# Kernel tuning notes

Hardware: AMD Instinct MI355X
Metric: run time of the kernel (lower is better)

## Reference

```python
import jax, jax.numpy as jnp
import numpy as np

EMBEDDING_DIM = 128
CODEBOOK_SIZE = 8192
COMMITMENT_COST = 0.25


def setup_inputs() -> dict:
    key = jax.random.key(0)
    k1, k2 = jax.random.split(key)
    inputs = jax.random.normal(k1, (8, 2048, EMBEDDING_DIM), dtype=jnp.float32)
    embeddings = jax.random.normal(k2, (EMBEDDING_DIM, CODEBOOK_SIZE), dtype=jnp.float32)
    return {"inputs": inputs, "embeddings": embeddings}


def reference(inputs, embeddings):
    # inputs: [B, T, D]; embeddings: [D, K]
    B, T, D = inputs.shape
    K = embeddings.shape[1]
    flat = inputs.reshape(-1, D)                      # [N, D]
    sim = flat @ embeddings                           # [N, K]
    dists = (jnp.sum(flat * flat, axis=1, keepdims=True)
             - 2.0 * sim
             + jnp.sum(embeddings * embeddings, axis=0, keepdims=True))
    idx_flat = jnp.argmax(-dists, axis=1)             # [N], matches tf.argmax(-d)
    encodings = jax.nn.one_hot(idx_flat, K, dtype=inputs.dtype)  # [N, K]
    encoding_indices = idx_flat.reshape(B, T)
    quantized = jnp.take(embeddings.T, encoding_indices, axis=0)  # [B, T, D]
    e_latent_loss = jnp.mean((jax.lax.stop_gradient(quantized) - inputs) ** 2)
    q_latent_loss = jnp.mean((quantized - jax.lax.stop_gradient(inputs)) ** 2)
    loss = q_latent_loss + COMMITMENT_COST * e_latent_loss
    quantized = inputs + jax.lax.stop_gradient(quantized - inputs)  # straight-through
    return quantized, encodings, encoding_indices, loss
```

## Files before the change

### kernel.cpp

```cpp
#include <hip/hip_runtime.h>

#define D 128
#define K 8192
#define N 16384
#define BM 64
#define BN 256
#define NCH (K / BN)
#define THREADS 512
#define CAND_CAP 3072
#define DELTA 0.5f
#define RMIN_INIT 0xFF800000u

typedef __attribute__((ext_vector_type(4))) float f32x4;
typedef __attribute__((ext_vector_type(16))) float f32x16;
typedef __attribute__((ext_vector_type(8))) short short8;

__device__ __forceinline__ unsigned short f2bf(float f) {
    unsigned int b = __float_as_uint(f);
    return (unsigned short)((b + 0x7FFFu + ((b >> 16) & 1u)) >> 16);
}
__device__ __forceinline__ unsigned int fsort(float f) {
    unsigned int b = __float_as_uint(f);
    return b ^ ((unsigned int)((int)b >> 31) | 0x80000000u);
}
__device__ __forceinline__ float funsort(unsigned int u) {
    return __uint_as_float((u & 0x80000000u) ? (u ^ 0x80000000u) : ~u);
}

__global__ __launch_bounds__(256) void prep_kernel(const float* __restrict__ E,
        unsigned short* __restrict__ e1t, float* __restrict__ e2t,
        float* __restrict__ enorm) {
    __shared__ float esum[8][32];
    const int t = threadIdx.x;
    const int kl = t & 31, dg = t >> 5;
    const int k = blockIdx.x * 32 + kl;
    float s = 0.f;
    __align__(16) unsigned short tmpb[16];
    __align__(16) float tmpf[16];
#pragma unroll
    for (int j = 0; j < 16; ++j) {
        float v = E[(size_t)(dg * 16 + j) * K + k];
        s += v * v;
        tmpb[j] = f2bf(v);
        tmpf[j] = v;
    }
    *(f32x4*)(e1t + (size_t)k * D + dg * 16) = *(const f32x4*)tmpb;
    *(f32x4*)(e1t + (size_t)k * D + dg * 16 + 8) = *(const f32x4*)(tmpb + 8);
    if (e2t) {
#pragma unroll
        for (int q = 0; q < 4; ++q)
            *(f32x4*)(e2t + (size_t)k * D + dg * 16 + 4 * q) = *(const f32x4*)(tmpf + 4 * q);
    }
    esum[dg][kl] = s;
    __syncthreads();
    if (t < 32) {
        float e = 0.f;
#pragma unroll
        for (int g = 0; g < 8; ++g) e += esum[g][t];
        enorm[blockIdx.x * 32 + t] = e;
    }
}

template<int E2T>
__global__ __launch_bounds__(THREADS, 2) void main_kernel(
        const float* __restrict__ X, const float* __restrict__ E,
        const unsigned short* __restrict__ e1t, const float* __restrict__ e2t,
        const float* __restrict__ enorm, float* __restrict__ out,
        float* __restrict__ partials) {
    __shared__ __align__(16) unsigned short b_s[2][BN * D];
    __shared__ unsigned long long cand[CAND_CAP];
    __shared__ unsigned long long best[BM];
    __shared__ unsigned int rmin[BM];
    __shared__ float red[THREADS];
    __shared__ int candn;

    const int t = threadIdx.x;
    const int wid = t >> 6, l = t & 63;
    const int l31 = l & 31, lh = l >> 5;
    const int wm = wid >> 2, wn = wid & 3;
    const int rowbase = blockIdx.x * BM;

    float* qout = out;
    float* enc = out + (size_t)N * D;
    float* idxout = enc + (size_t)N * K;

    if (t < BM) { rmin[t] = RMIN_INIT; best[t] = ~0ull; }
    if (t == 0) candn = 0;

    short8 afr[8];
    {
        const int row = rowbase + wm * 32 + l31;
#pragma unroll
        for (int ks = 0; ks < 8; ++ks) {
            const float* xp = X + (size_t)row * D + ks * 16 + lh * 8;
            f32x4 v0 = *(const f32x4*)xp;
            f32x4 v1 = *(const f32x4*)(xp + 4);
            short8 a;
            a[0] = (short)f2bf(v0[0]); a[1] = (short)f2bf(v0[1]);
            a[2] = (short)f2bf(v0[2]); a[3] = (short)f2bf(v0[3]);
            a[4] = (short)f2bf(v1[0]); a[5] = (short)f2bf(v1[1]);
            a[6] = (short)f2bf(v1[2]); a[7] = (short)f2bf(v1[3]);
            afr[ks] = a;
        }
    }

    f32x4 sreg[8];
    {
        const f32x4* gs = (const f32x4*)e1t;
#pragma unroll
        for (int i = 0; i < 8; ++i) sreg[i] = gs[t + THREADS * i];
#pragma unroll
        for (int i = 0; i < 8; ++i) {
            int unit = t + THREADS * i;
            int c = unit >> 4, slot = unit & 15;
            *(f32x4*)((char*)&b_s[0][0] + c * 256 + ((slot ^ (c & 15)) << 4)) = sreg[i];
        }
    }

    int cur = 0;
    for (int ch = 0; ch < NCH; ++ch) {
        if (ch + 1 < NCH) {
            const f32x4* gs = (const f32x4*)(e1t + (size_t)(ch + 1) * BN * D);
#pragma unroll
            for (int i = 0; i < 8; ++i) sreg[i] = gs[t + THREADS * i];
        }
        __syncthreads();

        float thrv[16];
#pragma unroll
        for (int q = 0; q < 4; ++q) {
            const int base = wm * 32 + 4 * lh + 8 * q;
            uint4 rv = *(const uint4*)&rmin[base];
            thrv[4 * q + 0] = funsort(rv.x);
            thrv[4 * q + 1] = funsort(rv.y);
            thrv[4 * q + 2] = funsort(rv.z);
            thrv[4 * q + 3] = funsort(rv.w);
        }

        f32x16 acc[2];
#pragma unroll
        for (int nf = 0; nf < 2; ++nf)
#pragma unroll
            for (int r = 0; r < 16; ++r) acc[nf][r] = 0.f;

#pragma unroll
        for (int ks = 0; ks < 8; ++ks) {
            short8 bf[2];
#pragma unroll
            for (int nf = 0; nf < 2; ++nf) {
                int c = wn * 64 + nf * 32 + l31;
                int slot = ks * 2 + lh;
                bf[nf] = *(const short8*)((const char*)&b_s[cur][0] + c * 256 + ((slot ^ (c & 15)) << 4));
            }
#pragma unroll
            for (int nf = 0; nf < 2; ++nf)
                acc[nf] = __builtin_amdgcn_mfma_f32_32x32x16_bf16(afr[ks], bf[nf], acc[nf], 0, 0, 0);
        }

        const int chcol = ch * BN;
        float dts[2][16];
#pragma unroll
        for (int nf = 0; nf < 2; ++nf) {
            const int col = chcol + wn * 64 + nf * 32 + l31;
            const float en = enorm[col];
#pragma unroll
            for (int r = 0; r < 16; ++r) dts[nf][r] = en - 2.f * acc[nf][r];
        }

        float cmin[16];
#pragma unroll
        for (int r = 0; r < 16; ++r) cmin[r] = fminf(dts[0][r], dts[1][r]);
#pragma unroll
        for (int m = 1; m <= 16; m <<= 1)
#pragma unroll
            for (int r = 0; r < 16; ++r)
                cmin[r] = fminf(cmin[r], __shfl_xor(cmin[r], m, 64));

#pragma unroll
        for (int r = 0; r < 16; ++r) {
            const int ro = wm * 32 + 4 * lh + 8 * (r >> 2) + (r & 3);
            const float te = fminf(thrv[r], cmin[r]) + DELTA;
#pragma unroll
            for (int nf = 0; nf < 2; ++nf) {
                if (dts[nf][r] < te) {
                    const int col = chcol + wn * 64 + nf * 32 + l31;
                    int ci = atomicAdd(&candn, 1);
                    if (ci < CAND_CAP)
                        cand[ci] = ((unsigned long long)fsort(dts[nf][r]) << 32) |
                                   ((unsigned long long)ro << 13) | (unsigned)col;
                }
            }
            if (l31 == 0 && cmin[r] < thrv[r])
                atomicMin(&rmin[ro], fsort(cmin[r]));
        }

        {
            const f32x4 z = {0.f, 0.f, 0.f, 0.f};
#pragma unroll
            for (int i = 0; i < 8; ++i) {
                int unit = t + THREADS * i;
                int row = unit >> 6, cu = unit & 63;
                __builtin_nontemporal_store(z,
                    (f32x4*)(enc + (size_t)(rowbase + row) * K + chcol + cu * 4));
            }
        }

        if (ch + 1 < NCH) {
#pragma unroll
            for (int i = 0; i < 8; ++i) {
                int unit = t + THREADS * i;
                int c = unit >> 4, slot = unit & 15;
                *(f32x4*)((char*)&b_s[cur ^ 1][0] + c * 256 + ((slot ^ (c & 15)) << 4)) = sreg[i];
            }
        }
        cur ^= 1;
    }

    __syncthreads();

    {
        int n = candn; if (n > CAND_CAP) n = CAND_CAP;
        for (int i = wid; i < n; i += 8) {
            const unsigned long long e = cand[i];
            const float dta = funsort((unsigned int)(e >> 32));
            const int ro = (int)((e >> 13) & 63u);
            const int col = (int)(e & 8191u);
            if (dta < funsort(rmin[ro]) + DELTA) {
                const int row = rowbase + ro;
                float x0 = X[(size_t)row * D + l];
                float x1 = X[(size_t)row * D + 64 + l];
                float e0, e1;
                if (E2T) {
                    e0 = e2t[(size_t)col * D + l];
                    e1 = e2t[(size_t)col * D + 64 + l];
                } else {
                    e0 = E[(size_t)l * K + col];
                    e1 = E[(size_t)(l + 64) * K + col];
                }
                float s = x0 * e0 + x1 * e1;
#pragma unroll
                for (int m = 1; m <= 32; m <<= 1) s += __shfl_xor(s, m, 64);
                if (l == 0) {
                    float dtx = enorm[col] - 2.f * s;
                    atomicMin(&best[ro],
                        ((unsigned long long)fsort(dtx) << 32) | (unsigned)col);
                }
            }
        }
    }
    __syncthreads();

    if (t < BM) {
        const int k = (int)(best[t] & 8191ull);
        idxout[rowbase + t] = (float)k;
        __builtin_nontemporal_store(1.0f, &enc[(size_t)(rowbase + t) * K + k]);
    }

    const int rr = t >> 3, sL = t & 7;
    const int row = rowbase + rr;
    const int kb = (int)(best[rr] & 8191ull);
    float part = 0.f;
#pragma unroll
    for (int j = 0; j < 4; ++j) {
        const int d0 = sL * 16 + 4 * j;
        f32x4 xv = *(const f32x4*)(X + (size_t)row * D + d0);
        f32x4 ev;
        if (E2T) {
            ev = *(const f32x4*)(e2t + (size_t)kb * D + d0);
        } else {
#pragma unroll
            for (int u = 0; u < 4; ++u) ev[u] = E[(size_t)(d0 + u) * K + kb];
        }
        f32x4 qv;
#pragma unroll
        for (int u = 0; u < 4; ++u) {
            float df = ev[u] - xv[u];
            qv[u] = xv[u] + df;
            part += df * df;
        }
        *(f32x4*)(qout + (size_t)row * D + d0) = qv;
    }
    red[t] = part;
    __syncthreads();
#pragma unroll
    for (int off = THREADS / 2; off > 0; off >>= 1) {
        if (t < off) red[t] += red[t + off];
        __syncthreads();
    }
    if (t == 0) partials[blockIdx.x] = red[0];
}

__global__ __launch_bounds__(256) void loss_kernel(const float* __restrict__ partials,
                                                   float* __restrict__ out) {
    __shared__ float red[256];
    const int t = threadIdx.x;
    red[t] = partials[t];
    __syncthreads();
    for (int off = 128; off > 0; off >>= 1) {
        if (t < off) red[t] += red[t + off];
        __syncthreads();
    }
    if (t == 0) {
        float mean = red[0] / (float)((size_t)N * D);
        out[(size_t)N * D + (size_t)N * K + N] = mean + 0.25f * mean;
    }
}

extern "C" void kernel_launch(void* const* d_in, const int* in_sizes, int n_in,
                              void* d_out, int out_size, void* d_ws, size_t ws_size,
                              hipStream_t stream) {
    const float* X = (const float*)d_in[0];
    const float* E = (const float*)d_in[1];
    float* out = (float*)d_out;
    char* ws = (char*)d_ws;

    const size_t E1T_B = (size_t)K * D * 2;
    const size_t E2T_B = (size_t)K * D * 4;
    const bool use_e2t = ws_size >= E1T_B + E2T_B + 64 * 1024;

    unsigned short* e1t = (unsigned short*)ws;
    float* e2t; float* enorm; float* partials;
    if (use_e2t) {
        e2t = (float*)(ws + E1T_B);
        enorm = (float*)(ws + E1T_B + E2T_B);
        partials = enorm + K;
    } else {
        e2t = nullptr;
        enorm = (float*)(ws + E1T_B);
        partials = enorm + K;
    }

    hipLaunchKernelGGL(prep_kernel, dim3(K / 32), dim3(256), 0, stream,
                       E, e1t, e2t, enorm);
    if (use_e2t)
        hipLaunchKernelGGL((main_kernel<1>), dim3(N / BM), dim3(THREADS), 0, stream,
                           X, E, e1t, e2t, enorm, out, partials);
    else
        hipLaunchKernelGGL((main_kernel<0>), dim3(N / BM), dim3(THREADS), 0, stream,
                           X, E, e1t, e2t, enorm, out, partials);
    hipLaunchKernelGGL(loss_kernel, dim3(1), dim3(256), 0, stream, partials, out);
}
```

Before: 200.5 us.

## Drop LDS staging of codebook; load B fragments directly from global per wave

```diff
diff --git a/kernel.cpp b/kernel.cpp
--- a/kernel.cpp
+++ b/kernel.cpp
@@ -3,11 +3,11 @@
 #define D 128
 #define K 8192
 #define N 16384
-#define BM 64
-#define BN 256
-#define NCH (K / BN)
-#define THREADS 512
-#define CAND_CAP 3072
+#define BM 32
+#define TILES 64
+#define GRP 4
+#define THREADS 256
+#define CAND_CAP 1024
 #define DELTA 0.5f
 #define RMIN_INIT 0xFF800000u
 
@@ -67,7 +67,6 @@
         const unsigned short* __restrict__ e1t, const float* __restrict__ e2t,
         const float* __restrict__ enorm, float* __restrict__ out,
         float* __restrict__ partials) {
-    __shared__ __align__(16) unsigned short b_s[2][BN * D];
     __shared__ unsigned long long cand[CAND_CAP];
     __shared__ unsigned long long best[BM];
     __shared__ unsigned int rmin[BM];
@@ -77,7 +76,7 @@
     const int t = threadIdx.x;
     const int wid = t >> 6, l = t & 63;
     const int l31 = l & 31, lh = l >> 5;
-    const int wm = wid >> 2, wn = wid & 3;
+    const int wn = wid;
     const int rowbase = blockIdx.x * BM;
 
     float* qout = out;
@@ -86,10 +85,11 @@
 
     if (t < BM) { rmin[t] = RMIN_INIT; best[t] = ~0ull; }
     if (t == 0) candn = 0;
+    __syncthreads();
 
     short8 afr[8];
     {
-        const int row = rowbase + wm * 32 + l31;
+        const int row = rowbase + l31;
 #pragma unroll
         for (int ks = 0; ks < 8; ++ks) {
             const float* xp = X + (size_t)row * D + ks * 16 + lh * 8;
@@ -104,32 +104,58 @@
         }
     }
 
-    f32x4 sreg[8];
-    {
-        const f32x4* gs = (const f32x4*)e1t;
-#pragma unroll
-        for (int i = 0; i < 8; ++i) sreg[i] = gs[t + THREADS * i];
-#pragma unroll
-        for (int i = 0; i < 8; ++i) {
-            int unit = t + THREADS * i;
-            int c = unit >> 4, slot = unit & 15;
-            *(f32x4*)((char*)&b_s[0][0] + c * 256 + ((slot ^ (c & 15)) << 4)) = sreg[i];
-        }
-    }
-
-    int cur = 0;
-    for (int ch = 0; ch < NCH; ++ch) {
-        if (ch + 1 < NCH) {
-            const f32x4* gs = (const f32x4*)(e1t + (size_t)(ch + 1) * BN * D);
-#pragma unroll
-            for (int i = 0; i < 8; ++i) sreg[i] = gs[t + THREADS * i];
-        }
-        __syncthreads();
+    const f32x4 z = {0.f, 0.f, 0.f, 0.f};
+    const int srow = l >> 3, scol = (l & 7) * 4;
+
+    for (int cg = 0; cg < TILES / GRP; ++cg) {
+        f32x16 dsv[GRP];
+#pragma unroll
+        for (int g = 0; g < GRP; ++g) {
+            const int ti = cg * GRP + g;
+            const int col0 = ti * 128 + wn * 32;
+            const int c = col0 + l31;
+
+            short8 bf[8];
+            const unsigned short* bp = e1t + (size_t)c * D + lh * 8;
+#pragma unroll
+            for (int ks = 0; ks < 8; ++ks)
+                bf[ks] = *(const short8*)(bp + ks * 16);
+            const float en = enorm[c];
+            asm volatile("" ::: "memory");
+
+            if (cg > 0 || g > 0) {
+                const int pcol0 = col0 - 128;
+#pragma unroll
+                for (int i = 0; i < 4; ++i)
+                    __builtin_nontemporal_store(z,
+                        (f32x4*)(enc + (size_t)(rowbase + i * 8 + srow) * K + pcol0 + scol));
+            }
+
+#pragma unroll
+            for (int r = 0; r < 16; ++r) dsv[g][r] = 0.f;
+#pragma unroll
+            for (int ks = 0; ks < 8; ++ks)
+                dsv[g] = __builtin_amdgcn_mfma_f32_32x32x16_bf16(afr[ks], bf[ks], dsv[g], 0, 0, 0);
+#pragma unroll
+            for (int r = 0; r < 16; ++r)
+                dsv[g][r] = fmaf(-2.f, dsv[g][r], en);
+        }
+
+        float lmin[16];
+#pragma unroll
+        for (int r = 0; r < 16; ++r)
+            lmin[r] = fminf(fminf(dsv[0][r], dsv[1][r]),
+                            fminf(dsv[2][r], dsv[3][r]));
+#pragma unroll
+        for (int m = 1; m <= 16; m <<= 1)
+#pragma unroll
+            for (int r = 0; r < 16; ++r)
+                lmin[r] = fminf(lmin[r], __shfl_xor(lmin[r], m, 64));
 
         float thrv[16];
 #pragma unroll
         for (int q = 0; q < 4; ++q) {
-            const int base = wm * 32 + 4 * lh + 8 * q;
+            const int base = 8 * q + 4 * lh;
             uint4 rv = *(const uint4*)&rmin[base];
             thrv[4 * q + 0] = funsort(rv.x);
             thrv[4 * q + 1] = funsort(rv.y);
@@ -137,90 +163,38 @@
             thrv[4 * q + 3] = funsort(rv.w);
         }
 
-        f32x16 acc[2];
-#pragma unroll
-        for (int nf = 0; nf < 2; ++nf)
-#pragma unroll
-            for (int r = 0; r < 16; ++r) acc[nf][r] = 0.f;
-
-#pragma unroll
-        for (int ks = 0; ks < 8; ++ks) {
-            short8 bf[2];
-#pragma unroll
-            for (int nf = 0; nf < 2; ++nf) {
-                int c = wn * 64 + nf * 32 + l31;
-                int slot = ks * 2 + lh;
-                bf[nf] = *(const short8*)((const char*)&b_s[cur][0] + c * 256 + ((slot ^ (c & 15)) << 4));
-            }
-#pragma unroll
-            for (int nf = 0; nf < 2; ++nf)
-                acc[nf] = __builtin_amdgcn_mfma_f32_32x32x16_bf16(afr[ks], bf[nf], acc[nf], 0, 0, 0);
-        }
-
-        const int chcol = ch * BN;
-        float dts[2][16];
-#pragma unroll
-        for (int nf = 0; nf < 2; ++nf) {
-            const int col = chcol + wn * 64 + nf * 32 + l31;
-            const float en = enorm[col];
-#pragma unroll
-            for (int r = 0; r < 16; ++r) dts[nf][r] = en - 2.f * acc[nf][r];
-        }
-
-        float cmin[16];
-#pragma unroll
-        for (int r = 0; r < 16; ++r) cmin[r] = fminf(dts[0][r], dts[1][r]);
-#pragma unroll
-        for (int m = 1; m <= 16; m <<= 1)
-#pragma unroll
-            for (int r = 0; r < 16; ++r)
-                cmin[r] = fminf(cmin[r], __shfl_xor(cmin[r], m, 64));
-
 #pragma unroll
         for (int r = 0; r < 16; ++r) {
-            const int ro = wm * 32 + 4 * lh + 8 * (r >> 2) + (r & 3);
-            const float te = fminf(thrv[r], cmin[r]) + DELTA;
-#pragma unroll
-            for (int nf = 0; nf < 2; ++nf) {
-                if (dts[nf][r] < te) {
-                    const int col = chcol + wn * 64 + nf * 32 + l31;
+            const int ro = (r & 3) + 8 * (r >> 2) + 4 * lh;
+            const float te = fminf(thrv[r], lmin[r]) + DELTA;
+#pragma unroll
+            for (int g = 0; g < GRP; ++g) {
+                if (dsv[g][r] < te) {
+                    const int col = (cg * GRP + g) * 128 + wn * 32 + l31;
                     int ci = atomicAdd(&candn, 1);
                     if (ci < CAND_CAP)
-                        cand[ci] = ((unsigned long long)fsort(dts[nf][r]) << 32) |
+                        cand[ci] = ((unsigned long long)fsort(dsv[g][r]) << 32) |
                                    ((unsigned long long)ro << 13) | (unsigned)col;
                 }
             }
-            if (l31 == 0 && cmin[r] < thrv[r])
-                atomicMin(&rmin[ro], fsort(cmin[r]));
-        }
-
-        {
-            const f32x4 z = {0.f, 0.f, 0.f, 0.f};
-#pragma unroll
-            for (int i = 0; i < 8; ++i) {
-                int unit = t + THREADS * i;
-                int row = unit >> 6, cu = unit & 63;
-                __builtin_nontemporal_store(z,
-                    (f32x4*)(enc + (size_t)(rowbase + row) * K + chcol + cu * 4));
-            }
-        }
-
-        if (ch + 1 < NCH) {
-#pragma unroll
-            for (int i = 0; i < 8; ++i) {
-                int unit = t + THREADS * i;
-                int c = unit >> 4, slot = unit & 15;
-                *(f32x4*)((char*)&b_s[cur ^ 1][0] + c * 256 + ((slot ^ (c & 15)) << 4)) = sreg[i];
-            }
-        }
-        cur ^= 1;
+            if (l31 == 0 && lmin[r] < thrv[r])
+                atomicMin(&rmin[ro], fsort(lmin[r]));
+        }
+    }
+
+    {
+        const int pcol0 = (TILES - 1) * 128 + wn * 32;
+#pragma unroll
+        for (int i = 0; i < 4; ++i)
+            __builtin_nontemporal_store(z,
+                (f32x4*)(enc + (size_t)(rowbase + i * 8 + srow) * K + pcol0 + scol));
     }
 
     __syncthreads();
 
     {
         int n = candn; if (n > CAND_CAP) n = CAND_CAP;
-        for (int i = wid; i < n; i += 8) {
+        for (int i = wid; i < n; i += 4) {
             const unsigned long long e = cand[i];
             const float dta = funsort((unsigned int)(e >> 32));
             const int ro = (int)((e >> 13) & 63u);
@@ -294,7 +268,7 @@
                                                    float* __restrict__ out) {
     __shared__ float red[256];
     const int t = threadIdx.x;
-    red[t] = partials[t];
+    red[t] = partials[t] + partials[t + 256];
     __syncthreads();
     for (int off = 128; off > 0; off >>= 1) {
         if (t < off) red[t] += red[t + off];
```

Measured after the change: 177.0 us. 11.7% less time.
